# Kernel tuning notes

Hardware: AMD Instinct MI355X
Metric: run time of the kernel (lower is better)

Reference implementation:

```python
import jax, jax.numpy as jnp
from jax import lax
import numpy as np

DIM = 768
NUM_HEADS = 12
HEAD_DIM = DIM // NUM_HEADS
POOL = 8
LAM1_INIT = 0.5
LAM2_INIT = 0.5
EPS = 1e-6


def rmsnorm(x, w):
    # x / (||x||_2 / sqrt(d) + eps) * w
    d = x.shape[-1]
    rms = jnp.sqrt(jnp.sum(x * x, axis=-1, keepdims=True)) / jnp.sqrt(jnp.asarray(d, x.dtype))
    return x / (rms + EPS) * w


def setup_inputs() -> dict:
    key = jax.random.key(0)
    ks = jax.random.split(key, 10)
    B, H, W = 32, 32, 32
    N = H * W
    x = jax.random.normal(ks[0], (B, N, DIM), dtype=jnp.float32)
    Wqkv = jax.random.normal(ks[1], (3 * DIM, DIM), dtype=jnp.float32) * 0.02
    Wproj = jax.random.normal(ks[2], (DIM, DIM), dtype=jnp.float32) * 0.02
    bproj = jnp.zeros((DIM,), dtype=jnp.float32)
    Wpos = jax.random.normal(ks[3], (HEAD_DIM, HEAD_DIM), dtype=jnp.float32) * 0.02
    Wneg = jax.random.normal(ks[4], (HEAD_DIM, HEAD_DIM), dtype=jnp.float32) * 0.02
    conv_w = jax.random.normal(ks[5], (HEAD_DIM, 1, 3, 3), dtype=jnp.float32) * 0.1  # depthwise OIHW
    lam1 = jnp.asarray(LAM1_INIT, dtype=jnp.float32)
    lam2 = jnp.asarray(LAM2_INIT, dtype=jnp.float32)
    norm1_w = jnp.ones((HEAD_DIM,), dtype=jnp.float32)
    norm2_w = jnp.ones((HEAD_DIM,), dtype=jnp.float32)
    return {"x": x, "Wqkv": Wqkv, "Wproj": Wproj, "bproj": bproj, "Wpos": Wpos,
            "Wneg": Wneg, "conv_w": conv_w, "lam1": lam1, "lam2": lam2,
            "norm1_w": norm1_w, "norm2_w": norm2_w, "H": H, "W": W}


def reference(x, Wqkv, Wproj, bproj, Wpos, Wneg, conv_w, lam1, lam2, norm1_w, norm2_w, H, W):
    B, N, C = x.shape
    h, hd, p = NUM_HEADS, HEAD_DIM, POOL
    scale = hd ** -0.5
    # qkv projection -> [3, B, h, N, hd]
    qkv = (x @ Wqkv.T).reshape(B, N, 3, h, hd).transpose(2, 0, 3, 1, 4)
    q, k, v = qkv[0], qkv[1], qkv[2]
    # depthwise conv + GELU on q in spatial form
    q2 = q.reshape(B, h, H, W, hd).transpose(0, 1, 4, 2, 3).reshape(B * h, hd, H, W)
    qe = lax.conv_general_dilated(q2, conv_w, window_strides=(1, 1), padding='SAME',
                                  feature_group_count=hd,
                                  dimension_numbers=('NCHW', 'OIHW', 'NCHW'))
    qe = jax.nn.gelu(qe, approximate=False)
    # adaptive avg pool to (p, p): exact since H % p == 0
    qp = qe.reshape(B * h, hd, p, H // p, p, W // p).mean(axis=(3, 5))
    t_base = qp.reshape(B, h, hd, p, p).transpose(0, 1, 3, 4, 2).reshape(B, h, p * p, hd)
    # dynamic e+/e- embeddings from global query
    gq = q.mean(axis=2)  # [B, h, hd]
    t_pos = t_base + (gq @ Wpos.T)[:, :, None, :]
    t_neg = t_base + (gq @ Wneg.T)[:, :, None, :]
    # stage 1: pooled contrast tokens attend to k/v
    attn_pos = jax.nn.softmax(jnp.einsum('bhmd,bhnd->bhmn', t_pos, k) * scale, axis=-1)
    v_hat_pos = attn_pos @ v  # [B, h, p*p, hd]
    attn_neg = jax.nn.softmax(jnp.einsum('bhmd,bhnd->bhmn', t_neg, k) * scale, axis=-1)
    v_hat_neg = attn_neg @ v
    v_contrast = rmsnorm(v_hat_pos - lam1 * v_hat_neg, norm1_w) * (1.0 - LAM1_INIT)
    # stage 2: q attends to contrast tokens
    attn1 = jax.nn.softmax(jnp.einsum('bhnd,bhmd->bhnm', q, t_pos) * scale, axis=-1)
    attn2 = jax.nn.softmax(jnp.einsum('bhnd,bhmd->bhnm', q, t_neg) * scale, axis=-1)
    out_patch = (attn1 - lam2 * attn2) @ v_contrast  # [B, h, N, hd]
    out_patch = rmsnorm(out_patch, norm2_w) * (1.0 - LAM2_INIT)
    out_patch = out_patch.transpose(0, 2, 1, 3).reshape(B, N, C)
    out = out_patch @ Wproj.T + bproj
    return out
```

## Files before the change

### kernel.cpp

```cpp
#include <hip/hip_runtime.h>
#include <hip/hip_bf16.h>


typedef __attribute__((ext_vector_type(8))) short short8;
typedef __attribute__((ext_vector_type(4))) short bf16x4;
typedef __attribute__((ext_vector_type(4))) float f32x4;

#define DEV static __device__ __forceinline__

DEV unsigned short f2bf(float f) {
  unsigned int b; __builtin_memcpy(&b, &f, 4);
  unsigned int r = (b + 0x7FFFu + ((b >> 16) & 1u)) >> 16;
  return (unsigned short)r;
}
DEV float bf2f(unsigned short u) {
  unsigned int b = ((unsigned int)u) << 16;
  float f; __builtin_memcpy(&f, &b, 4);
  return f;
}

DEV void gload16(const unsigned short* g, unsigned short* l) {
  __builtin_amdgcn_global_load_lds(
      (const __attribute__((address_space(1))) unsigned int*)g,
      (__attribute__((address_space(3))) unsigned int*)l, 16, 0, 0);
}

DEV void bar() {
  asm volatile("" ::: "memory");
  __builtin_amdgcn_s_barrier();
  asm volatile("" ::: "memory");
}
DEV void wait_vm4() { asm volatile("s_waitcnt vmcnt(4)" ::: "memory"); __builtin_amdgcn_sched_barrier(0); }
DEV void wait_vm0() { asm volatile("s_waitcnt vmcnt(0)" ::: "memory"); __builtin_amdgcn_sched_barrier(0); }

constexpr size_t SZ_QKV = (size_t)32 * 12 * 1024 * 64 * 2;
constexpr size_t OFF_Q   = 0;
constexpr size_t OFF_K   = OFF_Q + SZ_QKV;
constexpr size_t OFF_VT  = OFF_K + SZ_QKV;
constexpr size_t OFF_TPB = OFF_VT + SZ_QKV;
constexpr size_t OFF_TNB = OFF_TPB + 3145728;
constexpr size_t OFF_VCT = OFF_TNB + 3145728;
constexpr size_t OFF_OP  = OFF_VCT + 6291456;
constexpr size_t OFF_XB  = OFF_OP + SZ_QKV;
constexpr size_t OFF_WQ  = OFF_XB + SZ_QKV;
constexpr size_t OFF_WP  = OFF_WQ + 3538944;
constexpr size_t OFF_EP  = OFF_WP + 1179648;
constexpr size_t OFF_EN  = OFF_EP + 98304;

__global__ __launch_bounds__(256) void cast_kernel(const float* __restrict__ src,
                                                   unsigned short* __restrict__ dst, int n4) {
  int i = blockIdx.x * 256 + threadIdx.x;
  if (i >= n4) return;
  float4 v = reinterpret_cast<const float4*>(src)[i];
  ushort4 o;
  o.x = f2bf(v.x); o.y = f2bf(v.y); o.z = f2bf(v.z); o.w = f2bf(v.w);
  reinterpret_cast<ushort4*>(dst)[i] = o;
}

DEV void stage_ht(const unsigned short* __restrict__ G, unsigned short* shbase,
                  int grow0, int k0, int htrow0, int w, int lane) {
  const int rl = lane >> 3;
  const int ck = (lane & 7) ^ rl;
  const unsigned short* s0 = G + (size_t)(grow0 + htrow0 + w * 16 + rl) * 768 + k0 + ck * 8;
  gload16(s0, shbase + (htrow0 + w * 16) * 64);
  gload16(s0 + (size_t)8 * 768, shbase + (htrow0 + w * 16 + 8) * 64);
}

__global__ __launch_bounds__(512, 2) void gemm_qkv_kernel(const unsigned short* __restrict__ A,
    const unsigned short* __restrict__ Bm, unsigned short* __restrict__ q,
    unsigned short* __restrict__ k, unsigned short* __restrict__ vt) {
  __shared__ __align__(16) unsigned short sh[65536];
  const int t = threadIdx.x;
  const int lane = t & 63;
  const int w = t >> 6;
  const int wm = w >> 2, wn = w & 3;
  const int l = lane & 15, g = lane >> 4;
  const int id = blockIdx.x;
  const int swz = (id & 7) * 144 + (id >> 3);
  const int rt = swz / 9, ct = swz % 9;
  const int row0 = rt * 256, col0 = ct * 256;

  f32x4 acc[8][4];
#pragma unroll
  for (int i = 0; i < 8; ++i)
#pragma unroll
    for (int j = 0; j < 4; ++j) acc[i][j] = (f32x4){0.f, 0.f, 0.f, 0.f};

  stage_ht(A, sh, row0, 0, 0, w, lane);
  stage_ht(A, sh, row0, 0, 128, w, lane);
  stage_ht(Bm, sh + 32768, col0, 0, 0, w, lane);
  stage_ht(Bm, sh + 32768, col0, 0, 128, w, lane);
  stage_ht(Bm, sh + 32768 + 16384, col0, 64, 0, w, lane);
  stage_ht(Bm, sh + 32768 + 16384, col0, 64, 128, w, lane);
  wait_vm4();
  bar();

  for (int m = 0; m < 12; ++m) {
    const int d = m & 1;
    const unsigned short* Ab = sh + d * 16384;
    const unsigned short* Bb = sh + 32768 + d * 16384;
    short8 af[4][2], bf0[2][2], bf1[2][2];
#pragma unroll
    for (int mt = 0; mt < 4; ++mt)
#pragma unroll
      for (int kc = 0; kc < 2; ++kc) {
        const int r = wm * 128 + 0 * 64 + mt * 16 + l;
        af[mt][kc] = *reinterpret_cast<const short8*>(Ab + r * 64 + (((kc << 2) | g) ^ (r & 7)) * 8);
      }
#pragma unroll
    for (int nt = 0; nt < 2; ++nt)
#pragma unroll
      for (int kc = 0; kc < 2; ++kc) {
        const int r = wn * 64 + 0 * 32 + nt * 16 + l;
        bf0[nt][kc] = *reinterpret_cast<const short8*>(Bb + r * 64 + (((kc << 2) | g) ^ (r & 7)) * 8);
      }
    if (m + 1 < 12) stage_ht(A, sh + (d ^ 1) * 16384, row0, (m + 1) * 64, 0, w, lane);
    bar();
    __builtin_amdgcn_s_setprio(1);
#pragma unroll
    for (int kc = 0; kc < 2; ++kc)
#pragma unroll
      for (int mt = 0; mt < 4; ++mt)
#pragma unroll
        for (int nt = 0; nt < 2; ++nt)
          acc[mt][nt] = __builtin_amdgcn_mfma_f32_16x16x32_bf16(af[mt][kc], bf0[nt][kc], acc[mt][nt], 0, 0, 0);
    __builtin_amdgcn_s_setprio(0);
    bar();
#pragma unroll
    for (int nt = 0; nt < 2; ++nt)
#pragma unroll
      for (int kc = 0; kc < 2; ++kc) {
        const int r = wn * 64 + 32 + nt * 16 + l;
        bf1[nt][kc] = *reinterpret_cast<const short8*>(Bb + r * 64 + (((kc << 2) | g) ^ (r & 7)) * 8);
      }
    if (m + 1 < 12) stage_ht(A, sh + (d ^ 1) * 16384, row0, (m + 1) * 64, 128, w, lane);
    bar();
    __builtin_amdgcn_s_setprio(1);
#pragma unroll
    for (int kc = 0; kc < 2; ++kc)
#pragma unroll
      for (int mt = 0; mt < 4; ++mt)
#pragma unroll
        for (int nt = 0; nt < 2; ++nt)
          acc[mt][2 + nt] = __builtin_amdgcn_mfma_f32_16x16x32_bf16(af[mt][kc], bf1[nt][kc], acc[mt][2 + nt], 0, 0, 0);
    __builtin_amdgcn_s_setprio(0);
    bar();
#pragma unroll
    for (int mt = 0; mt < 4; ++mt)
#pragma unroll
      for (int kc = 0; kc < 2; ++kc) {
        const int r = wm * 128 + 64 + mt * 16 + l;
        af[mt][kc] = *reinterpret_cast<const short8*>(Ab + r * 64 + (((kc << 2) | g) ^ (r & 7)) * 8);
      }
    if (m + 2 < 12) stage_ht(Bm, sh + 32768 + d * 16384, col0, (m + 2) * 64, 0, w, lane);
    bar();
    __builtin_amdgcn_s_setprio(1);
#pragma unroll
    for (int kc = 0; kc < 2; ++kc)
#pragma unroll
      for (int mt = 0; mt < 4; ++mt)
#pragma unroll
        for (int nt = 0; nt < 2; ++nt)
          acc[4 + mt][2 + nt] = __builtin_amdgcn_mfma_f32_16x16x32_bf16(af[mt][kc], bf1[nt][kc], acc[4 + mt][2 + nt], 0, 0, 0);
    __builtin_amdgcn_s_setprio(0);
    bar();
    if (m + 2 < 12) stage_ht(Bm, sh + 32768 + d * 16384, col0, (m + 2) * 64, 128, w, lane);
    bar();
    __builtin_amdgcn_s_setprio(1);
#pragma unroll
    for (int kc = 0; kc < 2; ++kc)
#pragma unroll
      for (int mt = 0; mt < 4; ++mt)
#pragma unroll
        for (int nt = 0; nt < 2; ++nt)
          acc[4 + mt][nt] = __builtin_amdgcn_mfma_f32_16x16x32_bf16(af[mt][kc], bf0[nt][kc], acc[4 + mt][nt], 0, 0, 0);
    __builtin_amdgcn_s_setprio(0);
    if (m < 11) {
      if (m == 10) wait_vm0(); else wait_vm4();
    }
    bar();
  }

  const int s_ = ct / 3;
  if (s_ == 2) {
#pragma unroll
    for (int ni = 0; ni < 4; ++ni) {
      const int colg = (ct % 3) * 256 + wn * 64 + ni * 16 + l;
      const int head = colg >> 6, dd = colg & 63;
#pragma unroll
      for (int mi = 0; mi < 8; ++mi) {
        const int row = row0 + wm * 128 + mi * 16 + (g << 2);
        const int b = row >> 10, n = row & 1023;
        ushort4 pk;
        pk.x = f2bf(acc[mi][ni][0]); pk.y = f2bf(acc[mi][ni][1]);
        pk.z = f2bf(acc[mi][ni][2]); pk.w = f2bf(acc[mi][ni][3]);
        *reinterpret_cast<ushort4*>(vt + ((((size_t)b * 12 + head) * 64 + dd) << 10) + n) = pk;
      }
    }
  } else {
    unsigned short* dst = (s_ == 0) ? q : k;
#pragma unroll
    for (int ni = 0; ni < 4; ++ni) {
      const int colg = (ct % 3) * 256 + wn * 64 + ni * 16 + l;
      const int head = colg >> 6, dd = colg & 63;
#pragma unroll
      for (int mi = 0; mi < 8; ++mi) {
#pragma unroll
        for (int r = 0; r < 4; ++r) {
          const int row = row0 + wm * 128 + mi * 16 + (g << 2) + r;
          const int b = row >> 10, n = row & 1023;
          dst[(((size_t)b * 12 + head) * 1024 + n) * 64 + dd] = f2bf(acc[mi][ni][r]);
        }
      }
    }
  }
}

__global__ __launch_bounds__(256) void gq_embed_kernel(const unsigned short* __restrict__ qg,
    const float* __restrict__ Wpos, const float* __restrict__ Wneg,
    float* __restrict__ ep, float* __restrict__ en) {
  const int bh = blockIdx.x;
  const unsigned short* qp = qg + (size_t)bh * 65536;
  __shared__ float red2[32][64];
  __shared__ float gq_s[64];
  const int t = threadIdx.x;
  const int c8 = (t & 7) << 3;
  const int part = t >> 3;
  float s[8] = {0.f, 0.f, 0.f, 0.f, 0.f, 0.f, 0.f, 0.f};
  for (int i = 0; i < 32; ++i) {
    const short8 v = *reinterpret_cast<const short8*>(qp + (size_t)(part * 32 + i) * 64 + c8);
#pragma unroll
    for (int j = 0; j < 8; ++j) s[j] += bf2f((unsigned short)v[j]);
  }
#pragma unroll
  for (int j = 0; j < 8; ++j) red2[part][c8 + j] = s[j];
  __syncthreads();
  if (t < 64) {
    float s2 = 0.f;
    for (int p = 0; p < 32; ++p) s2 += red2[p][t];
    gq_s[t] = s2 * (1.0f / 1024.0f);
  }
  __syncthreads();
  if (t < 128) {
    const int d2 = t & 63;
    const float* Wm = (t < 64) ? Wpos : Wneg;
    float e = 0.f;
    for (int dd = 0; dd < 64; ++dd) e += gq_s[dd] * Wm[d2 * 64 + dd];
    (t < 64 ? ep : en)[bh * 64 + d2] = e;
  }
}

__global__ __launch_bounds__(256) void conv_pool_kernel(const unsigned short* __restrict__ qg,
    const float* __restrict__ conv_w, const float* __restrict__ ep,
    const float* __restrict__ en, unsigned short* __restrict__ t_pos,
    unsigned short* __restrict__ t_neg) {
  const int bh = blockIdx.x;
  const int quad = blockIdx.y;
  const unsigned short* qp = qg + (size_t)bh * 65536;
  __shared__ float pool_s[16][64];
  const int t = threadIdx.x;
  const int dg = t & 7, sp = t >> 3;
  const int d0 = dg << 3;
  float cw[3][3][8];
#pragma unroll
  for (int ky = 0; ky < 3; ++ky)
#pragma unroll
    for (int kx = 0; kx < 3; ++kx)
#pragma unroll
      for (int j = 0; j < 8; ++j)
        cw[ky][kx][j] = conv_w[(d0 + j) * 9 + ky * 3 + kx];
#pragma unroll
  for (int pyl = 0; pyl < 2; ++pyl) {
    float win[8] = {0.f, 0.f, 0.f, 0.f, 0.f, 0.f, 0.f, 0.f};
#pragma unroll
    for (int iy = 0; iy < 4; ++iy) {
      const int y = quad * 8 + pyl * 4 + iy;
      float a[8] = {0.f, 0.f, 0.f, 0.f, 0.f, 0.f, 0.f, 0.f};
#pragma unroll
      for (int ky = 0; ky < 3; ++ky) {
        const int yy = y + ky - 1;
        if (yy < 0 || yy > 31) continue;
#pragma unroll
        for (int kx = 0; kx < 3; ++kx) {
          const int xx = sp + kx - 1;
          if (xx < 0 || xx > 31) continue;
          const short8 v = *reinterpret_cast<const short8*>(qp + (size_t)(yy * 32 + xx) * 64 + d0);
#pragma unroll
          for (int j = 0; j < 8; ++j) a[j] += bf2f((unsigned short)v[j]) * cw[ky][kx][j];
        }
      }
#pragma unroll
      for (int j = 0; j < 8; ++j)
        win[j] += 0.5f * a[j] * (1.0f + erff(a[j] * 0.70710678118654752440f));
    }
#pragma unroll
    for (int j = 0; j < 8; ++j) {
      win[j] += __shfl_xor(win[j], 8);
      win[j] += __shfl_xor(win[j], 16);
    }
    if ((sp & 3) == 0) {
      const int px = sp >> 2;
#pragma unroll
      for (int j = 0; j < 8; ++j) pool_s[pyl * 8 + px][d0 + j] = win[j];
    }
  }
  __syncthreads();
#pragma unroll
  for (int i = 0; i < 4; ++i) {
    const int idx = i * 256 + t;
    const int m = idx >> 6, dd = idx & 63;
    const int mg = quad * 16 + m;
    const float base = pool_s[m][dd] * (1.0f / 16.0f);
    t_pos[(size_t)bh * 4096 + mg * 64 + dd] = f2bf(base + ep[bh * 64 + dd]);
    t_neg[(size_t)bh * 4096 + mg * 64 + dd] = f2bf(base + en[bh * 64 + dd]);
  }
}

__global__ __launch_bounds__(256) void stage1_kernel(const unsigned short* __restrict__ kg,
    const unsigned short* __restrict__ vtg, const unsigned short* __restrict__ tpb,
    const unsigned short* __restrict__ tnb, const float* __restrict__ lam1p,
    const float* __restrict__ norm1_w, float* __restrict__ vct) {
  const int bh = blockIdx.x;
  __shared__ unsigned short tp[64 * 72], tn[64 * 72];
  __shared__ unsigned short Ks[64 * 72], Vts[64 * 72];
  const int t = threadIdx.x;
  const int lane = t & 63;
  const int w = t >> 6;
  const int l = lane & 15, g = lane >> 4;
  for (int L = t; L < 512; L += 256) {
    const int r = L >> 3, c = (L & 7) << 3;
    *reinterpret_cast<short8*>(tp + r * 72 + c) =
        *reinterpret_cast<const short8*>(tpb + (size_t)bh * 4096 + r * 64 + c);
    *reinterpret_cast<short8*>(tn + r * 72 + c) =
        *reinterpret_cast<const short8*>(tnb + (size_t)bh * 4096 + r * 64 + c);
  }
  __syncthreads();
  short8 tf[2][2];
#pragma unroll
  for (int h = 0; h < 2; ++h) {
    tf[0][h] = *reinterpret_cast<const short8*>(tp + (w * 16 + l) * 72 + h * 32 + g * 8);
    tf[1][h] = *reinterpret_cast<const short8*>(tn + (w * 16 + l) * 72 + h * 32 + g * 8);
  }
  float Mo[2] = {-1e30f, -1e30f}, Lo[2] = {0.f, 0.f};
  f32x4 acc[2][4];
#pragma unroll
  for (int pp = 0; pp < 2; ++pp)
#pragma unroll
    for (int dt = 0; dt < 4; ++dt) acc[pp][dt] = (f32x4){0.f, 0.f, 0.f, 0.f};
  const size_t kbase = (size_t)bh * 65536;

  for (int n0 = 0; n0 < 1024; n0 += 64) {
    __syncthreads();
    for (int L = t; L < 512; L += 256) {
      const int r = L >> 3, c = (L & 7) << 3;
      *reinterpret_cast<short8*>(Ks + r * 72 + c) =
          *reinterpret_cast<const short8*>(kg + kbase + (size_t)(n0 + r) * 64 + c);
      *reinterpret_cast<short8*>(Vts + r * 72 + c) =
          *reinterpret_cast<const short8*>(vtg + kbase + (size_t)r * 1024 + n0 + c);
    }
    __syncthreads();
    short8 kf[4][2];
#pragma unroll
    for (int tile = 0; tile < 4; ++tile)
#pragma unroll
      for (int h = 0; h < 2; ++h)
        kf[tile][h] = *reinterpret_cast<const short8*>(Ks + (tile * 16 + l) * 72 + h * 32 + g * 8);
    bf16x4 pf[2][4];
#pragma unroll
    for (int pp = 0; pp < 2; ++pp) {
      f32x4 s[4];
#pragma unroll
      for (int tile = 0; tile < 4; ++tile) {
        s[tile] = (f32x4){0.f, 0.f, 0.f, 0.f};
#pragma unroll
        for (int h = 0; h < 2; ++h)
          s[tile] = __builtin_amdgcn_mfma_f32_16x16x32_bf16(kf[tile][h], tf[pp][h], s[tile], 0, 0, 0);
      }
      float p[4][4];
      float tmax = -1e30f;
#pragma unroll
      for (int tile = 0; tile < 4; ++tile)
#pragma unroll
        for (int r = 0; r < 4; ++r) {
          const float v = s[tile][r] * 0.125f;
          p[tile][r] = v;
          tmax = fmaxf(tmax, v);
        }
      tmax = fmaxf(tmax, __shfl_xor(tmax, 16));
      tmax = fmaxf(tmax, __shfl_xor(tmax, 32));
      const float nm = fmaxf(Mo[pp], tmax);
      const float al = __expf(Mo[pp] - nm);
      Mo[pp] = nm;
      float ps = 0.f;
#pragma unroll
      for (int tile = 0; tile < 4; ++tile)
#pragma unroll
        for (int r = 0; r < 4; ++r) {
          const float e = __expf(p[tile][r] - nm);
          p[tile][r] = e;
          ps += e;
        }
      ps += __shfl_xor(ps, 16);
      ps += __shfl_xor(ps, 32);
      Lo[pp] = Lo[pp] * al + ps;
#pragma unroll
      for (int tile = 0; tile < 4; ++tile) {
        bf16x4 pk;
        pk[0] = (short)f2bf(p[tile][0]); pk[1] = (short)f2bf(p[tile][1]);
        pk[2] = (short)f2bf(p[tile][2]); pk[3] = (short)f2bf(p[tile][3]);
        pf[pp][tile] = pk;
      }
      float ar[4];
#pragma unroll
      for (int r = 0; r < 4; ++r) ar[r] = __shfl(al, 4 * g + r);
#pragma unroll
      for (int dt = 0; dt < 4; ++dt)
#pragma unroll
        for (int r = 0; r < 4; ++r) acc[pp][dt][r] *= ar[r];
    }
#pragma unroll
    for (int tile = 0; tile < 4; ++tile)
#pragma unroll
      for (int dt = 0; dt < 4; ++dt) {
        const bf16x4 vf = *reinterpret_cast<const bf16x4*>(Vts + (dt * 16 + l) * 72 + tile * 16 + g * 4);
        acc[0][dt] = __builtin_amdgcn_mfma_f32_16x16x16bf16_1k(pf[0][tile], vf, acc[0][dt], 0, 0, 0);
        acc[1][dt] = __builtin_amdgcn_mfma_f32_16x16x16bf16_1k(pf[1][tile], vf, acc[1][dt], 0, 0, 0);
      }
  }
  const float inv0 = 1.f / Lo[0], inv1 = 1.f / Lo[1];
  float i1r[4], i2r[4];
#pragma unroll
  for (int r = 0; r < 4; ++r) {
    i1r[r] = __shfl(inv0, 4 * g + r);
    i2r[r] = __shfl(inv1, 4 * g + r);
  }
  const float lam1 = lam1p[0];
  float od[4][4], ss[4] = {0.f, 0.f, 0.f, 0.f};
#pragma unroll
  for (int dt = 0; dt < 4; ++dt)
#pragma unroll
    for (int r = 0; r < 4; ++r) {
      const float v = acc[0][dt][r] * i1r[r] - lam1 * (acc[1][dt][r] * i2r[r]);
      od[dt][r] = v;
      ss[r] += v * v;
    }
#pragma unroll
  for (int r = 0; r < 4; ++r) {
    ss[r] += __shfl_xor(ss[r], 1);
    ss[r] += __shfl_xor(ss[r], 2);
    ss[r] += __shfl_xor(ss[r], 4);
    ss[r] += __shfl_xor(ss[r], 8);
  }
  float sc[4];
#pragma unroll
  for (int r = 0; r < 4; ++r) sc[r] = 0.5f / (sqrtf(ss[r]) * 0.125f + 1e-6f);
  const int mb = w * 16 + 4 * g;
#pragma unroll
  for (int dt = 0; dt < 4; ++dt) {
    const int dd = dt * 16 + l;
    const float nw = norm1_w[dd];
#pragma unroll
    for (int r = 0; r < 4; ++r)
      vct[(size_t)bh * 4096 + dd * 64 + mb + r] = od[dt][r] * sc[r] * nw;
  }
}

__global__ __launch_bounds__(256) void stage2_kernel(const unsigned short* __restrict__ qg,
    const unsigned short* __restrict__ tpb, const unsigned short* __restrict__ tnb,
    const float* __restrict__ vct, const float* __restrict__ lam2p,
    const float* __restrict__ norm2_w, unsigned short* __restrict__ opb) {
  const int bh = blockIdx.x;
  const int q0 = blockIdx.y * 64;
  __shared__ unsigned short tp[64 * 72], tn[64 * 72], Qs[64 * 72], Vc[64 * 72];
  const int t = threadIdx.x;
  const int lane = t & 63;
  const int w = t >> 6;
  const int l = lane & 15, g = lane >> 4;
  for (int L = t; L < 512; L += 256) {
    const int r = L >> 3, c = (L & 7) << 3;
    *reinterpret_cast<short8*>(tp + r * 72 + c) =
        *reinterpret_cast<const short8*>(tpb + (size_t)bh * 4096 + r * 64 + c);
    *reinterpret_cast<short8*>(tn + r * 72 + c) =
        *reinterpret_cast<const short8*>(tnb + (size_t)bh * 4096 + r * 64 + c);
    *reinterpret_cast<short8*>(Qs + r * 72 + c) =
        *reinterpret_cast<const short8*>(qg + (size_t)bh * 65536 + (size_t)(q0 + r) * 64 + c);
  }
  for (int L = t; L < 4096; L += 256) {
    const int dd = L >> 6, m = L & 63;
    Vc[dd * 72 + m] = f2bf(vct[(size_t)bh * 4096 + L]);
  }
  __syncthreads();
  short8 qf[2];
#pragma unroll
  for (int h = 0; h < 2; ++h)
    qf[h] = *reinterpret_cast<const short8*>(Qs + (w * 16 + l) * 72 + h * 32 + g * 8);
  bf16x4 vcf[4][4];
#pragma unroll
  for (int tile = 0; tile < 4; ++tile)
#pragma unroll
    for (int dt = 0; dt < 4; ++dt)
      vcf[tile][dt] = *reinterpret_cast<const bf16x4*>(Vc + (dt * 16 + l) * 72 + tile * 16 + g * 4);
  bf16x4 pf[2][4];
#pragma unroll
  for (int pp = 0; pp < 2; ++pp) {
    const unsigned short* tm = pp ? tn : tp;
    f32x4 s[4];
#pragma unroll
    for (int tile = 0; tile < 4; ++tile) {
      s[tile] = (f32x4){0.f, 0.f, 0.f, 0.f};
#pragma unroll
      for (int h = 0; h < 2; ++h) {
        const short8 tfb = *reinterpret_cast<const short8*>(tm + (tile * 16 + l) * 72 + h * 32 + g * 8);
        s[tile] = __builtin_amdgcn_mfma_f32_16x16x32_bf16(tfb, qf[h], s[tile], 0, 0, 0);
      }
    }
    float p[4][4];
    float lmax = -1e30f;
#pragma unroll
    for (int tile = 0; tile < 4; ++tile)
#pragma unroll
      for (int r = 0; r < 4; ++r) {
        const float v = s[tile][r] * 0.125f;
        p[tile][r] = v;
        lmax = fmaxf(lmax, v);
      }
    lmax = fmaxf(lmax, __shfl_xor(lmax, 16));
    lmax = fmaxf(lmax, __shfl_xor(lmax, 32));
    float ps = 0.f;
#pragma unroll
    for (int tile = 0; tile < 4; ++tile)
#pragma unroll
      for (int r = 0; r < 4; ++r) {
        const float e = __expf(p[tile][r] - lmax);
        p[tile][r] = e;
        ps += e;
      }
    ps += __shfl_xor(ps, 16);
    ps += __shfl_xor(ps, 32);
    const float inv = 1.f / ps;
#pragma unroll
    for (int tile = 0; tile < 4; ++tile) {
      bf16x4 pk;
      pk[0] = (short)f2bf(p[tile][0] * inv); pk[1] = (short)f2bf(p[tile][1] * inv);
      pk[2] = (short)f2bf(p[tile][2] * inv); pk[3] = (short)f2bf(p[tile][3] * inv);
      pf[pp][tile] = pk;
    }
  }
  f32x4 a1[4], a2[4];
#pragma unroll
  for (int dt = 0; dt < 4; ++dt) {
    a1[dt] = (f32x4){0.f, 0.f, 0.f, 0.f};
    a2[dt] = (f32x4){0.f, 0.f, 0.f, 0.f};
  }
#pragma unroll
  for (int tile = 0; tile < 4; ++tile)
#pragma unroll
    for (int dt = 0; dt < 4; ++dt) {
      a1[dt] = __builtin_amdgcn_mfma_f32_16x16x16bf16_1k(pf[0][tile], vcf[tile][dt], a1[dt], 0, 0, 0);
      a2[dt] = __builtin_amdgcn_mfma_f32_16x16x16bf16_1k(pf[1][tile], vcf[tile][dt], a2[dt], 0, 0, 0);
    }
  const float lam2 = lam2p[0];
  float od[4][4], ss[4] = {0.f, 0.f, 0.f, 0.f};
#pragma unroll
  for (int dt = 0; dt < 4; ++dt)
#pragma unroll
    for (int r = 0; r < 4; ++r) {
      const float v = a1[dt][r] - lam2 * a2[dt][r];
      od[dt][r] = v;
      ss[r] += v * v;
    }
#pragma unroll
  for (int r = 0; r < 4; ++r) {
    ss[r] += __shfl_xor(ss[r], 1);
    ss[r] += __shfl_xor(ss[r], 2);
    ss[r] += __shfl_xor(ss[r], 4);
    ss[r] += __shfl_xor(ss[r], 8);
  }
  float sc[4];
#pragma unroll
  for (int r = 0; r < 4; ++r) sc[r] = 0.5f / (sqrtf(ss[r]) * 0.125f + 1e-6f);
  const int b = bh / 12, head = bh % 12;
  const size_t ob = ((size_t)b * 1024 + q0 + w * 16 + 4 * g) * 768 + head * 64;
#pragma unroll
  for (int dt = 0; dt < 4; ++dt) {
    const float nw = norm2_w[dt * 16 + l];
#pragma unroll
    for (int r = 0; r < 4; ++r)
      opb[ob + (size_t)r * 768 + dt * 16 + l] = f2bf(od[dt][r] * sc[r] * nw);
  }
}

DEV void stage_tile(const unsigned short* __restrict__ A,
                    const unsigned short* __restrict__ Bm,
                    unsigned short* As, unsigned short* Bs,
                    int row0, int col0, int k0, int w, int srow, int scol) {
#pragma unroll
  for (int kc = 0; kc < 2; ++kc)
#pragma unroll
    for (int j = 0; j < 2; ++j) {
      const int qs = w * 2 + j;
      const int r = qs * 16 + srow;
      const int cg = k0 + kc * 32 + scol;
      gload16(A + (size_t)(row0 + r) * 768 + cg, As + kc * 4096 + qs * 512);
      gload16(Bm + (size_t)(col0 + r) * 768 + cg, Bs + kc * 4096 + qs * 512);
    }
}

__global__ __launch_bounds__(256) void gemm_proj_kernel(const unsigned short* __restrict__ A,
    const unsigned short* __restrict__ Bm, const float* __restrict__ bias,
    float* __restrict__ out) {
  __shared__ unsigned short As[2][8192];
  __shared__ unsigned short Bs[2][8192];
  const int t = threadIdx.x;
  const int lane = t & 63;
  const int w = t >> 6;
  const int wm = w >> 1, wn = w & 1;
  const int id = blockIdx.x;
  const int swz = (id & 7) * 192 + (id >> 3);
  const int row0 = (swz / 6) * 128;
  const int col0 = (swz % 6) * 128;
  f32x4 acc[4][4];
#pragma unroll
  for (int i = 0; i < 4; ++i)
#pragma unroll
    for (int j = 0; j < 4; ++j) acc[i][j] = (f32x4){0.f, 0.f, 0.f, 0.f};
  const int l = lane & 15, g = lane >> 4;
  const int srow = lane >> 2, scol = (lane & 3) << 3;

  stage_tile(A, Bm, As[0], Bs[0], row0, col0, 0, w, srow, scol);
  __syncthreads();
  for (int kt = 0; kt < 12; ++kt) {
    const int cur = kt & 1;
    if (kt < 11)
      stage_tile(A, Bm, As[cur ^ 1], Bs[cur ^ 1], row0, col0, (kt + 1) * 64, w, srow, scol);
#pragma unroll
    for (int kc = 0; kc < 2; ++kc) {
      short8 af[4], bfv[4];
#pragma unroll
      for (int mt = 0; mt < 4; ++mt)
        af[mt] = *reinterpret_cast<const short8*>(As[cur] + kc * 4096 + (wm * 64 + mt * 16 + l) * 32 + g * 8);
#pragma unroll
      for (int nt = 0; nt < 4; ++nt)
        bfv[nt] = *reinterpret_cast<const short8*>(Bs[cur] + kc * 4096 + (wn * 64 + nt * 16 + l) * 32 + g * 8);
#pragma unroll
      for (int mt = 0; mt < 4; ++mt)
#pragma unroll
        for (int nt = 0; nt < 4; ++nt)
          acc[mt][nt] = __builtin_amdgcn_mfma_f32_16x16x32_bf16(af[mt], bfv[nt], acc[mt][nt], 0, 0, 0);
    }
    __syncthreads();
  }
#pragma unroll
  for (int nt = 0; nt < 4; ++nt) {
    const int col = col0 + wn * 64 + nt * 16 + l;
    const float bv = bias[col];
#pragma unroll
    for (int mt = 0; mt < 4; ++mt)
#pragma unroll
      for (int r = 0; r < 4; ++r) {
        const int row = row0 + wm * 64 + mt * 16 + (g << 2) + r;
        out[(size_t)row * 768 + col] = acc[mt][nt][r] + bv;
      }
  }
}

extern "C" void kernel_launch(void* const* d_in, const int* in_sizes, int n_in,
                              void* d_out, int out_size, void* d_ws, size_t ws_size,
                              hipStream_t stream) {
  (void)in_sizes; (void)n_in; (void)out_size; (void)ws_size;
  const float* x       = (const float*)d_in[0];
  const float* Wqkv    = (const float*)d_in[1];
  const float* Wproj   = (const float*)d_in[2];
  const float* bproj   = (const float*)d_in[3];
  const float* Wpos    = (const float*)d_in[4];
  const float* Wneg    = (const float*)d_in[5];
  const float* conv_w  = (const float*)d_in[6];
  const float* lam1    = (const float*)d_in[7];
  const float* lam2    = (const float*)d_in[8];
  const float* norm1_w = (const float*)d_in[9];
  const float* norm2_w = (const float*)d_in[10];
  float* out = (float*)d_out;
  char* ws = (char*)d_ws;
  unsigned short* qb   = (unsigned short*)(ws + OFF_Q);
  unsigned short* kb   = (unsigned short*)(ws + OFF_K);
  unsigned short* vtb  = (unsigned short*)(ws + OFF_VT);
  unsigned short* tpbb = (unsigned short*)(ws + OFF_TPB);
  unsigned short* tnbb = (unsigned short*)(ws + OFF_TNB);
  float* vctb          = (float*)(ws + OFF_VCT);
  unsigned short* opb  = (unsigned short*)(ws + OFF_OP);
  unsigned short* xb   = (unsigned short*)(ws + OFF_XB);
  unsigned short* wqb  = (unsigned short*)(ws + OFF_WQ);
  unsigned short* wpb  = (unsigned short*)(ws + OFF_WP);
  float* epb           = (float*)(ws + OFF_EP);
  float* enb           = (float*)(ws + OFF_EN);

  cast_kernel<<<dim3(6291456 / 256), dim3(256), 0, stream>>>(x, xb, 6291456);
  cast_kernel<<<dim3(442368 / 256), dim3(256), 0, stream>>>(Wqkv, wqb, 442368);
  cast_kernel<<<dim3(147456 / 256), dim3(256), 0, stream>>>(Wproj, wpb, 147456);
  gemm_qkv_kernel<<<dim3(1152), dim3(512), 0, stream>>>(xb, wqb, qb, kb, vtb);
  gq_embed_kernel<<<dim3(384), dim3(256), 0, stream>>>(qb, Wpos, Wneg, epb, enb);
  conv_pool_kernel<<<dim3(384, 4), dim3(256), 0, stream>>>(qb, conv_w, epb, enb, tpbb, tnbb);
  stage1_kernel<<<dim3(384), dim3(256), 0, stream>>>(kb, vtb, tpbb, tnbb, lam1, norm1_w, vctb);
  stage2_kernel<<<dim3(384, 16), dim3(256), 0, stream>>>(qb, tpbb, tnbb, vctb, lam2, norm2_w, opb);
  gemm_proj_kernel<<<dim3(1536), dim3(256), 0, stream>>>(opb, wpb, bproj, out);
}
```

Baseline: 435.2 us.

## Double-buffer stage1 KV loads, emit bf16 contrast values, retile projection GEMM

Stage1 now stages K and V^T tiles through direct global-to-LDS loads into swizzled double buffers, so the next tile's fetch overlaps the current tile's compute. Stage1 also writes v_contrast as packed bf16 instead of fp32, which lets stage2 load it with vector copies rather than converting element by element. The projection GEMM moves to 128x256 tiles with 512 threads, using the same split-B prefetch pipeline as the QKV GEMM. These changes add tighter wait and barrier choreography and round v_contrast to bf16 one step earlier.

After: 389.4 us. 1.12x faster.

```diff
diff --git a/kernel.cpp b/kernel.cpp
--- a/kernel.cpp
+++ b/kernel.cpp
@@ -32,6 +32,7 @@
 }
 DEV void wait_vm4() { asm volatile("s_waitcnt vmcnt(4)" ::: "memory"); __builtin_amdgcn_sched_barrier(0); }
 DEV void wait_vm0() { asm volatile("s_waitcnt vmcnt(0)" ::: "memory"); __builtin_amdgcn_sched_barrier(0); }
+DEV void wait_lgkm0() { asm volatile("s_waitcnt lgkmcnt(0)" ::: "memory"); __builtin_amdgcn_sched_barrier(0); }
 
 constexpr size_t SZ_QKV = (size_t)32 * 12 * 1024 * 64 * 2;
 constexpr size_t OFF_Q   = 0;
@@ -104,14 +105,14 @@
     for (int mt = 0; mt < 4; ++mt)
 #pragma unroll
       for (int kc = 0; kc < 2; ++kc) {
-        const int r = wm * 128 + 0 * 64 + mt * 16 + l;
+        const int r = wm * 128 + mt * 16 + l;
         af[mt][kc] = *reinterpret_cast<const short8*>(Ab + r * 64 + (((kc << 2) | g) ^ (r & 7)) * 8);
       }
 #pragma unroll
     for (int nt = 0; nt < 2; ++nt)
 #pragma unroll
       for (int kc = 0; kc < 2; ++kc) {
-        const int r = wn * 64 + 0 * 32 + nt * 16 + l;
+        const int r = wn * 64 + nt * 16 + l;
         bf0[nt][kc] = *reinterpret_cast<const short8*>(Bb + r * 64 + (((kc << 2) | g) ^ (r & 7)) * 8);
       }
     if (m + 1 < 12) stage_ht(A, sh + (d ^ 1) * 16384, row0, (m + 1) * 64, 0, w, lane);
@@ -319,14 +320,18 @@
 __global__ __launch_bounds__(256) void stage1_kernel(const unsigned short* __restrict__ kg,
     const unsigned short* __restrict__ vtg, const unsigned short* __restrict__ tpb,
     const unsigned short* __restrict__ tnb, const float* __restrict__ lam1p,
-    const float* __restrict__ norm1_w, float* __restrict__ vct) {
+    const float* __restrict__ norm1_w, unsigned short* __restrict__ vct) {
   const int bh = blockIdx.x;
   __shared__ unsigned short tp[64 * 72], tn[64 * 72];
-  __shared__ unsigned short Ks[64 * 72], Vts[64 * 72];
+  __shared__ __align__(16) unsigned short Ks[2][4096];
+  __shared__ __align__(16) unsigned short Vts[2][4096];
   const int t = threadIdx.x;
   const int lane = t & 63;
   const int w = t >> 6;
   const int l = lane & 15, g = lane >> 4;
+  const size_t kbase = (size_t)bh * 65536;
+  const int rl = lane >> 3, ck = (lane & 7) ^ rl;
+
   for (int L = t; L < 512; L += 256) {
     const int r = L >> 3, c = (L & 7) << 3;
     *reinterpret_cast<short8*>(tp + r * 72 + c) =
@@ -334,7 +339,17 @@
     *reinterpret_cast<short8*>(tn + r * 72 + c) =
         *reinterpret_cast<const short8*>(tnb + (size_t)bh * 4096 + r * 64 + c);
   }
+  auto stageKV = [&](int buf, int n0) {
+    const unsigned short* ksrc = kg + kbase + (size_t)(n0 + w * 16 + rl) * 64 + ck * 8;
+    gload16(ksrc, &Ks[buf][(w * 16) * 64]);
+    gload16(ksrc + (size_t)8 * 64, &Ks[buf][(w * 16 + 8) * 64]);
+    const unsigned short* vsrc = vtg + kbase + (size_t)(w * 16 + rl) * 1024 + n0 + ck * 8;
+    gload16(vsrc, &Vts[buf][(w * 16) * 64]);
+    gload16(vsrc + (size_t)8 * 1024, &Vts[buf][(w * 16 + 8) * 64]);
+  };
+  stageKV(0, 0);
   __syncthreads();
+
   short8 tf[2][2];
 #pragma unroll
   for (int h = 0; h < 2; ++h) {
@@ -347,24 +362,18 @@
   for (int pp = 0; pp < 2; ++pp)
 #pragma unroll
     for (int dt = 0; dt < 4; ++dt) acc[pp][dt] = (f32x4){0.f, 0.f, 0.f, 0.f};
-  const size_t kbase = (size_t)bh * 65536;
-
-  for (int n0 = 0; n0 < 1024; n0 += 64) {
-    __syncthreads();
-    for (int L = t; L < 512; L += 256) {
-      const int r = L >> 3, c = (L & 7) << 3;
-      *reinterpret_cast<short8*>(Ks + r * 72 + c) =
-          *reinterpret_cast<const short8*>(kg + kbase + (size_t)(n0 + r) * 64 + c);
-      *reinterpret_cast<short8*>(Vts + r * 72 + c) =
-          *reinterpret_cast<const short8*>(vtg + kbase + (size_t)r * 1024 + n0 + c);
-    }
-    __syncthreads();
+
+  for (int it = 0; it < 16; ++it) {
+    const int buf = it & 1;
+    if (it < 15) stageKV(buf ^ 1, (it + 1) * 64);
     short8 kf[4][2];
 #pragma unroll
     for (int tile = 0; tile < 4; ++tile)
 #pragma unroll
-      for (int h = 0; h < 2; ++h)
-        kf[tile][h] = *reinterpret_cast<const short8*>(Ks + (tile * 16 + l) * 72 + h * 32 + g * 8);
+      for (int h = 0; h < 2; ++h) {
+        const int R = tile * 16 + l;
+        kf[tile][h] = *reinterpret_cast<const short8*>(&Ks[buf][R * 64 + ((((h << 2) | g)) ^ (l & 7)) * 8]);
+      }
     bf16x4 pf[2][4];
 #pragma unroll
     for (int pp = 0; pp < 2; ++pp) {
@@ -422,10 +431,13 @@
     for (int tile = 0; tile < 4; ++tile)
 #pragma unroll
       for (int dt = 0; dt < 4; ++dt) {
-        const bf16x4 vf = *reinterpret_cast<const bf16x4*>(Vts + (dt * 16 + l) * 72 + tile * 16 + g * 4);
+        const int R = dt * 16 + l;
+        const bf16x4 vf = *reinterpret_cast<const bf16x4*>(
+            &Vts[buf][R * 64 + (((2 * tile + (g >> 1)) ^ (l & 7)) * 8) + (g & 1) * 4]);
         acc[0][dt] = __builtin_amdgcn_mfma_f32_16x16x16bf16_1k(pf[0][tile], vf, acc[0][dt], 0, 0, 0);
         acc[1][dt] = __builtin_amdgcn_mfma_f32_16x16x16bf16_1k(pf[1][tile], vf, acc[1][dt], 0, 0, 0);
       }
+    __syncthreads();
   }
   const float inv0 = 1.f / Lo[0], inv1 = 1.f / Lo[1];
   float i1r[4], i2r[4];
@@ -459,15 +471,18 @@
   for (int dt = 0; dt < 4; ++dt) {
     const int dd = dt * 16 + l;
     const float nw = norm1_w[dd];
-#pragma unroll
-    for (int r = 0; r < 4; ++r)
-      vct[(size_t)bh * 4096 + dd * 64 + mb + r] = od[dt][r] * sc[r] * nw;
+    ushort4 pk;
+    pk.x = f2bf(od[dt][0] * sc[0] * nw);
+    pk.y = f2bf(od[dt][1] * sc[1] * nw);
+    pk.z = f2bf(od[dt][2] * sc[2] * nw);
+    pk.w = f2bf(od[dt][3] * sc[3] * nw);
+    *reinterpret_cast<ushort4*>(vct + (size_t)bh * 4096 + dd * 64 + mb) = pk;
   }
 }
 
 __global__ __launch_bounds__(256) void stage2_kernel(const unsigned short* __restrict__ qg,
     const unsigned short* __restrict__ tpb, const unsigned short* __restrict__ tnb,
-    const float* __restrict__ vct, const float* __restrict__ lam2p,
+    const unsigned short* __restrict__ vctg, const float* __restrict__ lam2p,
     const float* __restrict__ norm2_w, unsigned short* __restrict__ opb) {
   const int bh = blockIdx.x;
   const int q0 = blockIdx.y * 64;
@@ -484,10 +499,8 @@
         *reinterpret_cast<const short8*>(tnb + (size_t)bh * 4096 + r * 64 + c);
     *reinterpret_cast<short8*>(Qs + r * 72 + c) =
         *reinterpret_cast<const short8*>(qg + (size_t)bh * 65536 + (size_t)(q0 + r) * 64 + c);
-  }
-  for (int L = t; L < 4096; L += 256) {
-    const int dd = L >> 6, m = L & 63;
-    Vc[dd * 72 + m] = f2bf(vct[(size_t)bh * 4096 + L]);
+    *reinterpret_cast<short8*>(Vc + r * 72 + c) =
+        *reinterpret_cast<const short8*>(vctg + (size_t)bh * 4096 + r * 64 + c);
   }
   __syncthreads();
   short8 qf[2];
@@ -590,76 +603,102 @@
   }
 }
 
-DEV void stage_tile(const unsigned short* __restrict__ A,
-                    const unsigned short* __restrict__ Bm,
-                    unsigned short* As, unsigned short* Bs,
-                    int row0, int col0, int k0, int w, int srow, int scol) {
-#pragma unroll
-  for (int kc = 0; kc < 2; ++kc)
-#pragma unroll
-    for (int j = 0; j < 2; ++j) {
-      const int qs = w * 2 + j;
-      const int r = qs * 16 + srow;
-      const int cg = k0 + kc * 32 + scol;
-      gload16(A + (size_t)(row0 + r) * 768 + cg, As + kc * 4096 + qs * 512);
-      gload16(Bm + (size_t)(col0 + r) * 768 + cg, Bs + kc * 4096 + qs * 512);
-    }
-}
-
-__global__ __launch_bounds__(256) void gemm_proj_kernel(const unsigned short* __restrict__ A,
+__global__ __launch_bounds__(512, 2) void gemm_proj_kernel(const unsigned short* __restrict__ A,
     const unsigned short* __restrict__ Bm, const float* __restrict__ bias,
     float* __restrict__ out) {
-  __shared__ unsigned short As[2][8192];
-  __shared__ unsigned short Bs[2][8192];
+  __shared__ __align__(16) unsigned short sh[49152];
   const int t = threadIdx.x;
   const int lane = t & 63;
   const int w = t >> 6;
-  const int wm = w >> 1, wn = w & 1;
+  const int wm = w >> 2, wn = w & 3;
+  const int l = lane & 15, g = lane >> 4;
   const int id = blockIdx.x;
-  const int swz = (id & 7) * 192 + (id >> 3);
-  const int row0 = (swz / 6) * 128;
-  const int col0 = (swz % 6) * 128;
+  const int swz = (id & 7) * 96 + (id >> 3);
+  const int rt = swz / 3, ct = swz % 3;
+  const int row0 = rt * 128, col0 = ct * 256;
+
   f32x4 acc[4][4];
 #pragma unroll
   for (int i = 0; i < 4; ++i)
 #pragma unroll
     for (int j = 0; j < 4; ++j) acc[i][j] = (f32x4){0.f, 0.f, 0.f, 0.f};
-  const int l = lane & 15, g = lane >> 4;
-  const int srow = lane >> 2, scol = (lane & 3) << 3;
-
-  stage_tile(A, Bm, As[0], Bs[0], row0, col0, 0, w, srow, scol);
-  __syncthreads();
-  for (int kt = 0; kt < 12; ++kt) {
-    const int cur = kt & 1;
-    if (kt < 11)
-      stage_tile(A, Bm, As[cur ^ 1], Bs[cur ^ 1], row0, col0, (kt + 1) * 64, w, srow, scol);
-#pragma unroll
-    for (int kc = 0; kc < 2; ++kc) {
-      short8 af[4], bfv[4];
+
+  stage_ht(A, sh, row0, 0, 0, w, lane);
+  stage_ht(Bm, sh + 16384, col0, 0, 0, w, lane);
+  stage_ht(Bm, sh + 16384, col0, 0, 128, w, lane);
+  stage_ht(Bm, sh + 32768, col0, 64, 0, w, lane);
+  stage_ht(Bm, sh + 32768, col0, 64, 128, w, lane);
+  wait_vm4();
+  bar();
+
+  for (int m = 0; m < 12; ++m) {
+    const int d = m & 1;
+    const unsigned short* Ab = sh + d * 8192;
+    const unsigned short* Bb = sh + 16384 + d * 16384;
+    short8 af[4][2], bfv[4][2];
+#pragma unroll
+    for (int mt = 0; mt < 4; ++mt)
+#pragma unroll
+      for (int kc = 0; kc < 2; ++kc) {
+        const int r = wm * 64 + mt * 16 + l;
+        af[mt][kc] = *reinterpret_cast<const short8*>(Ab + r * 64 + (((kc << 2) | g) ^ (r & 7)) * 8);
+      }
+#pragma unroll
+    for (int nt = 0; nt < 2; ++nt)
+#pragma unroll
+      for (int kc = 0; kc < 2; ++kc) {
+        const int r = wn * 64 + nt * 16 + l;
+        bfv[nt][kc] = *reinterpret_cast<const short8*>(Bb + r * 64 + (((kc << 2) | g) ^ (r & 7)) * 8);
+      }
+    if (m + 1 < 12) stage_ht(A, sh + (d ^ 1) * 8192, row0, (m + 1) * 64, 0, w, lane);
+    bar();
+    __builtin_amdgcn_s_setprio(1);
+#pragma unroll
+    for (int kc = 0; kc < 2; ++kc)
 #pragma unroll
       for (int mt = 0; mt < 4; ++mt)
-        af[mt] = *reinterpret_cast<const short8*>(As[cur] + kc * 4096 + (wm * 64 + mt * 16 + l) * 32 + g * 8);
-#pragma unroll
-      for (int nt = 0; nt < 4; ++nt)
-        bfv[nt] = *reinterpret_cast<const short8*>(Bs[cur] + kc * 4096 + (wn * 64 + nt * 16 + l) * 32 + g * 8);
+#pragma unroll
+        for (int nt = 0; nt < 2; ++nt)
+          acc[mt][nt] = __builtin_amdgcn_mfma_f32_16x16x32_bf16(af[mt][kc], bfv[nt][kc], acc[mt][nt], 0, 0, 0);
+    __builtin_amdgcn_s_setprio(0);
+    bar();
+#pragma unroll
+    for (int nt = 2; nt < 4; ++nt)
+#pragma unroll
+      for (int kc = 0; kc < 2; ++kc) {
+        const int r = wn * 64 + nt * 16 + l;
+        bfv[nt][kc] = *reinterpret_cast<const short8*>(Bb + r * 64 + (((kc << 2) | g) ^ (r & 7)) * 8);
+      }
+    wait_lgkm0();
+    bar();
+    if (m + 2 < 12) {
+      stage_ht(Bm, sh + 16384 + d * 16384, col0, (m + 2) * 64, 0, w, lane);
+      stage_ht(Bm, sh + 16384 + d * 16384, col0, (m + 2) * 64, 128, w, lane);
+    }
+    __builtin_amdgcn_s_setprio(1);
+#pragma unroll
+    for (int kc = 0; kc < 2; ++kc)
 #pragma unroll
       for (int mt = 0; mt < 4; ++mt)
 #pragma unroll
-        for (int nt = 0; nt < 4; ++nt)
-          acc[mt][nt] = __builtin_amdgcn_mfma_f32_16x16x32_bf16(af[mt], bfv[nt], acc[mt][nt], 0, 0, 0);
-    }
-    __syncthreads();
-  }
-#pragma unroll
-  for (int nt = 0; nt < 4; ++nt) {
-    const int col = col0 + wn * 64 + nt * 16 + l;
-    const float bv = bias[col];
-#pragma unroll
-    for (int mt = 0; mt < 4; ++mt)
+        for (int nt = 2; nt < 4; ++nt)
+          acc[mt][nt] = __builtin_amdgcn_mfma_f32_16x16x32_bf16(af[mt][kc], bfv[nt][kc], acc[mt][nt], 0, 0, 0);
+    __builtin_amdgcn_s_setprio(0);
+    if (m < 11) {
+      if (m == 10) wait_vm0(); else wait_vm4();
+    }
+    bar();
+  }
+#pragma unroll
+  for (int ni = 0; ni < 4; ++ni) {
+    const int colg = ct * 256 + wn * 64 + ni * 16 + l;
+    const float bv = bias[colg];
+#pragma unroll
+    for (int mi = 0; mi < 4; ++mi)
 #pragma unroll
       for (int r = 0; r < 4; ++r) {
-        const int row = row0 + wm * 64 + mt * 16 + (g << 2) + r;
-        out[(size_t)row * 768 + col] = acc[mt][nt][r] + bv;
+        const int row = row0 + wm * 64 + mi * 16 + (g << 2) + r;
+        out[(size_t)row * 768 + colg] = acc[mi][ni][r] + bv;
       }
   }
 }
@@ -686,7 +725,7 @@
   unsigned short* vtb  = (unsigned short*)(ws + OFF_VT);
   unsigned short* tpbb = (unsigned short*)(ws + OFF_TPB);
   unsigned short* tnbb = (unsigned short*)(ws + OFF_TNB);
-  float* vctb          = (float*)(ws + OFF_VCT);
+  unsigned short* vctb = (unsigned short*)(ws + OFF_VCT);
   unsigned short* opb  = (unsigned short*)(ws + OFF_OP);
   unsigned short* xb   = (unsigned short*)(ws + OFF_XB);
   unsigned short* wqb  = (unsigned short*)(ws + OFF_WQ);
@@ -702,5 +741,5 @@
   conv_pool_kernel<<<dim3(384, 4), dim3(256), 0, stream>>>(qb, conv_w, epb, enb, tpbb, tnbb);
   stage1_kernel<<<dim3(384), dim3(256), 0, stream>>>(kb, vtb, tpbb, tnbb, lam1, norm1_w, vctb);
   stage2_kernel<<<dim3(384, 16), dim3(256), 0, stream>>>(qb, tpbb, tnbb, vctb, lam2, norm2_w, opb);
-  gemm_proj_kernel<<<dim3(1536), dim3(256), 0, stream>>>(opb, wpb, bproj, out);
-}
+  gemm_proj_kernel<<<dim3(768), dim3(512), 0, stream>>>(opb, wpb, bproj, out);
+}
```
